# Kernel tuning notes

Hardware: AMD Instinct MI355X
Metric: run time of the kernel (lower is better)

Reference implementation:

```python
import jax
import jax.numpy as jnp
import numpy as np
from jax import lax

B, L, H, M = 32768, 128, 256, 16


def setup_inputs() -> dict:
    key = jax.random.key(0)
    ks = jax.random.split(key, 7)
    s_ih = 1.0 / np.sqrt(H)  # PyTorch GRUCell init scale (uniform bound); use scaled normal
    return {
        "x": jax.random.randint(ks[0], (B, L), 0, M, dtype=jnp.int32),
        "W_ih": jax.random.normal(ks[1], (3 * H, 1), dtype=jnp.float32) * s_ih,
        "W_hh": jax.random.normal(ks[2], (3 * H, H), dtype=jnp.float32) * s_ih,
        "b_ih": jax.random.normal(ks[3], (3 * H,), dtype=jnp.float32) * s_ih,
        "b_hh": jax.random.normal(ks[4], (3 * H,), dtype=jnp.float32) * s_ih,
        "W_fc": jax.random.normal(ks[5], (M, H), dtype=jnp.float32) * s_ih,
        "b_fc": jax.random.normal(ks[6], (M,), dtype=jnp.float32) * s_ih,
    }


def reference(x, W_ih, W_hh, b_ih, b_hh, W_fc, b_fc):
    # (zeros at i=0) as a scalar feature; output log_softmax gathered at x[:, i].
    xf = x.astype(jnp.float32)
    x_in = jnp.concatenate([jnp.zeros((x.shape[0], 1), jnp.float32), xf[:, :-1]], axis=1)  # [B, L]

    def step(h, inp):
        x_t, tgt = inp  # x_t: [B] float, tgt: [B] int
        gi = x_t[:, None] * W_ih.T + b_ih            # [B, 3H] (input dim is 1)
        gh = h @ W_hh.T + b_hh                       # [B, 3H]
        ir, iz, i_n = jnp.split(gi, 3, axis=1)
        hr, hz, h_n = jnp.split(gh, 3, axis=1)
        r = jax.nn.sigmoid(ir + hr)
        z = jax.nn.sigmoid(iz + hz)
        n = jnp.tanh(i_n + r * h_n)
        h_new = (1.0 - z) * n + z * h                # [B, H]
        logp = jax.nn.log_softmax(h_new @ W_fc.T + b_fc, axis=1)  # [B, M]
        lp = jnp.take_along_axis(logp, tgt[:, None], axis=1)[:, 0]  # [B]
        return h_new, lp

    h0 = jnp.zeros((x.shape[0], W_hh.shape[1]), jnp.float32)
    _, lps = lax.scan(step, h0, (x_in.T, x.T))  # lps: [L, B]
    return lps.sum(axis=0)  # [B] log_probsum
```

## Files before the change

### kernel.cpp

```cpp
#include <hip/hip_runtime.h>

typedef __attribute__((ext_vector_type(8))) short s16x8;
typedef __attribute__((ext_vector_type(4))) float f32x4;
typedef __attribute__((ext_vector_type(16))) float f32x16;

#define BATCH 32768
#define LSEQ 128
#define W32_SHORTS (8 * 4 * 17 * 512)
#define WFC_SHORTS 4096
#define XT_OFF_BYTES ((W32_SHORTS + WFC_SHORTS) * 2)
#define WS_NEED_XT (XT_OFF_BYTES + BATCH * LSEQ * 4)

#define HROW 264
#define HBUF_S (128 * HROW)
#define LDS_BYTES (2 * HBUF_S * 2 + 1024)

#define L2E 1.4426950408889634f
#define LN2 0.6931471805599453f

#define MFMA32(A, B, C) __builtin_amdgcn_mfma_f32_32x32x16_bf16(A, B, C, 0, 0, 0)
#define MFMA16(A, B, C) __builtin_amdgcn_mfma_f32_16x16x32_bf16(A, B, C, 0, 0, 0)

__device__ __forceinline__ unsigned short f2b(float f) {
  unsigned u = __float_as_uint(f);
  u += 0x7FFFu + ((u >> 16) & 1u);
  return (unsigned short)(u >> 16);
}

__device__ __forceinline__ float exp2n(float x) { float r; asm("v_exp_f32 %0, -%1" : "=v"(r) : "v"(x)); return r; }
__device__ __forceinline__ float exp2p(float x) { float r; asm("v_exp_f32 %0, %1" : "=v"(r) : "v"(x)); return r; }
__device__ __forceinline__ float rcp_(float x)  { float r; asm("v_rcp_f32 %0, %1" : "=v"(r) : "v"(x)); return r; }
__device__ __forceinline__ float log2_(float x) { float r; asm("v_log_f32 %0, %1" : "=v"(r) : "v"(x)); return r; }
__device__ __forceinline__ unsigned cvtpk(float lo, float hi) {
  unsigned r; asm("v_cvt_pk_bf16_f32 %0, %1, %2" : "=v"(r) : "v"(lo), "v"(hi)); return r;
}

__global__ void gru_prep(const float* __restrict__ Wih, const float* __restrict__ Whh,
                         const float* __restrict__ bih, const float* __restrict__ bhh,
                         const float* __restrict__ Wfc,
                         unsigned short* __restrict__ wfrag,
                         unsigned short* __restrict__ wfc16) {
  int t = blockIdx.x * 256 + threadIdx.x;
  if (t < W32_SHORTS) {
    int e = t & 7, lane = (t >> 3) & 63, frag = t >> 9;
    int ks = frag % 17, g = (frag / 17) & 3, tr = frag / 68;
    int l31 = lane & 31, hh = lane >> 5;
    int k = (ks < 16) ? ks * 16 + hh * 8 + e : 256 + hh * 8 + e;
    float val = 0.f;
    if (g < 3) {
      int j = g * 256 + tr * 32 + l31;
      if (k < 256) val = Whh[j * 256 + k];
      else if (k == 256) val = (g < 2) ? Wih[j] : 0.f;
      else if (k == 257) val = (g < 2) ? (bih[j] + bhh[j]) : bhh[j];
    }
    wfrag[t] = f2b(val);
  } else if (t < W32_SHORTS + WFC_SHORTS) {
    int t2 = t - W32_SHORTS;
    wfc16[t2] = f2b(Wfc[t2]);
  }
}

__global__ void x_transpose(const int* __restrict__ x, int* __restrict__ xT) {
  __shared__ int tile[32][33];
  int l0 = blockIdx.x * 32, b0 = blockIdx.y * 32;
  for (int r = threadIdx.y; r < 32; r += 8)
    tile[r][threadIdx.x] = x[(b0 + r) * LSEQ + l0 + threadIdx.x];
  __syncthreads();
  for (int r = threadIdx.y; r < 32; r += 8)
    xT[(l0 + r) * BATCH + b0 + threadIdx.x] = tile[threadIdx.x][r];
}

template <int XT>
__global__ __attribute__((amdgpu_waves_per_eu(2, 2))) __launch_bounds__(512)
void gru_main(const int* __restrict__ x, const int* __restrict__ xTr,
              const unsigned short* __restrict__ wfrag,
              const unsigned short* __restrict__ wfc16,
              const float* __restrict__ Wih, const float* __restrict__ bih,
              const float* __restrict__ bfc, float* __restrict__ out) {
  extern __shared__ unsigned short sm[];
  unsigned short* h0 = sm;
  unsigned short* h1 = sm + HBUF_S;
  unsigned* wl_in = (unsigned*)(sm + 2 * HBUF_S);

  const int tid = threadIdx.x;
  const int lane = tid & 63;
  const int wv = tid >> 6;
  const int tr = wv;
  const int l31 = lane & 31;
  const int hh = lane >> 5;
  const int q = lane >> 4;
  const int b = lane & 15;
  const int bbase = blockIdx.x * 128;

  {
    unsigned int* p = (unsigned int*)h0;
#pragma unroll
    for (int r = 0; r < 33; ++r) p[tid + r * 512] = 0u;
  }
  if (tid < 256) {
    int j = 512 + tid;
    wl_in[tid] = (unsigned)f2b(Wih[j]) | ((unsigned)f2b(bih[j]) << 16);
  }

  float bfc4[4];
#pragma unroll
  for (int r = 0; r < 4; ++r) bfc4[r] = bfc[q * 4 + r];

  const f32x16 z16 = {0, 0, 0, 0, 0, 0, 0, 0, 0, 0, 0, 0, 0, 0, 0, 0};

  float lp = 0.f;
  __syncthreads();

#pragma unroll 1
  for (int i = 0; i < LSEQ; ++i) {
    const unsigned short* rdb = (i & 1) ? h1 : h0;
    unsigned short* wrb = (i & 1) ? h0 : h1;

    unsigned long wfu = (unsigned long)wfrag;
    asm volatile("" : "+s"(wfu));
    const unsigned short* wfp = (const unsigned short*)wfu;
    unsigned long wcu = (unsigned long)wfc16;
    asm volatile("" : "+s"(wcu));
    const unsigned short* wc = (const unsigned short*)wcu;

    const unsigned short* fR = wfp + ((tr * 4 + 0) * 17) * 512 + lane * 8;
    const unsigned short* fZ = wfp + ((tr * 4 + 1) * 17) * 512 + lane * 8;
    const unsigned short* fH = wfp + ((tr * 4 + 2) * 17) * 512 + lane * 8;

    float xin4[4];
    unsigned xlo[4];
#pragma unroll
    for (int bg = 0; bg < 4; ++bg) {
      float xv;
      if (XT) xv = (i > 0) ? (float)xTr[(i - 1) * BATCH + bbase + bg * 32 + l31] : 0.f;
      else    xv = (i > 0) ? (float)x[(bbase + bg * 32 + l31) * LSEQ + i - 1] : 0.f;
      xin4[bg] = xv;
      xlo[bg] = (hh == 0) ? ((__float_as_uint(xv) >> 16) | 0x3F800000u) : 0u;
    }

    s16x8 ar = *(const s16x8*)(fR + 16 * 512);
    s16x8 az = *(const s16x8*)(fZ + 16 * 512);
    s16x8 ah = *(const s16x8*)(fH + 16 * 512);
    f32x16 aRc[4], aZc[4], aHc[4];
#pragma unroll
    for (int bg = 0; bg < 4; ++bg) {
      union { unsigned u[4]; s16x8 v; } xf;
      xf.u[0] = xlo[bg]; xf.u[1] = xf.u[2] = xf.u[3] = 0u;
      aRc[bg] = MFMA32(ar, xf.v, z16);
      aZc[bg] = MFMA32(az, xf.v, z16);
      aHc[bg] = MFMA32(ah, xf.v, z16);
    }

    const unsigned short* rbB = rdb + l31 * HROW + 8 * hh;

    s16x8 cr = *(const s16x8*)(fR);
    s16x8 cz = *(const s16x8*)(fZ);
    s16x8 ch = *(const s16x8*)(fH);
#pragma unroll
    for (int ks = 0; ks < 16; ++ks) {
      s16x8 nr, nz, nh;
      if (ks < 15) {
        nr = *(const s16x8*)(fR + (ks + 1) * 512);
        nz = *(const s16x8*)(fZ + (ks + 1) * 512);
        nh = *(const s16x8*)(fH + (ks + 1) * 512);
      }
#pragma unroll
      for (int bg = 0; bg < 4; ++bg) {
        const s16x8 hb = *(const s16x8*)&rbB[bg * 32 * HROW + ks * 16];
        aRc[bg] = MFMA32(cr, hb, aRc[bg]);
        aZc[bg] = MFMA32(cz, hb, aZc[bg]);
        aHc[bg] = MFMA32(ch, hb, aHc[bg]);
      }
      if (ks < 15) { cr = nr; cz = nz; ch = nh; }
    }

    const unsigned short* rbE = rdb + l31 * HROW + tr * 32 + 4 * hh;
    unsigned short* wbE = wrb + l31 * HROW + tr * 32 + 4 * hh;
    const unsigned* wlt = wl_in + tr * 32 + 4 * hh;
#pragma unroll
    for (int bg = 0; bg < 4; ++bg) {
      const float xv = xin4[bg];
#pragma unroll
      for (int rq = 0; rq < 4; ++rq) {
        const uint2 hp = *(const uint2*)&rbE[bg * 32 * HROW + 8 * rq];
        const float hpv[4] = {
            __uint_as_float(hp.x << 16), __uint_as_float(hp.x & 0xFFFF0000u),
            __uint_as_float(hp.y << 16), __uint_as_float(hp.y & 0xFFFF0000u)};
        float hv[4];
#pragma unroll
        for (int e2 = 0; e2 < 4; ++e2) {
          const int idx = rq * 4 + e2;
          const unsigned u = wlt[8 * rq + e2];
          const float inr = fmaf(xv, __uint_as_float(u << 16),
                                 __uint_as_float(u & 0xFFFF0000u));
          float rr = rcp_(1.f + exp2n(L2E * aRc[bg][idx]));
          float zz = rcp_(1.f + exp2n(L2E * aZc[bg][idx]));
          float y  = fmaf(rr, aHc[bg][idx], inr);
          float uu = rcp_(1.f + exp2p((2.f * L2E) * y));
          float nn = fmaf(-2.f, uu, 1.f);
          hv[e2] = fmaf(zz, hpv[e2] - nn, nn);
        }
        *(uint2*)&wbE[bg * 32 * HROW + 8 * rq] =
            make_uint2(cvtpk(hv[0], hv[1]), cvtpk(hv[2], hv[3]));
      }
    }

    __syncthreads();

    {
      const int lrow = wv * 16 + b;
      const int grow = bbase + lrow;
      f32x4 fa = {bfc4[0], bfc4[1], bfc4[2], bfc4[3]};
      const unsigned short* hbb = wrb + lrow * HROW + 8 * q;
      const unsigned short* wcb = wc + b * 256 + q * 8;
#pragma unroll
      for (int ks = 0; ks < 8; ++ks) {
        s16x8 wfcf = *(const s16x8*)(wcb + 32 * ks);
        s16x8 hb = *(const s16x8*)(hbb + 32 * ks);
        fa = MFMA16(wfcf, hb, fa);
      }
      int tgt = XT ? xTr[i * BATCH + grow] : x[grow * LSEQ + i];
      float l0 = fa[0], l1 = fa[1], l2 = fa[2], l3 = fa[3];
      float mx = fmaxf(fmaxf(l0, l1), fmaxf(l2, l3));
      mx = fmaxf(mx, __shfl_xor(mx, 16));
      mx = fmaxf(mx, __shfl_xor(mx, 32));
      float se = exp2p(L2E * (l0 - mx)) + exp2p(L2E * (l1 - mx)) +
                 exp2p(L2E * (l2 - mx)) + exp2p(L2E * (l3 - mx));
      se += __shfl_xor(se, 16);
      se += __shfl_xor(se, 32);
      float v01 = (tgt & 1) ? l1 : l0;
      float v23 = (tgt & 1) ? l3 : l2;
      float vs = (tgt & 2) ? v23 : v01;
      float contrib = (q == (tgt >> 2)) ? vs : 0.f;
      contrib += __shfl_xor(contrib, 16);
      contrib += __shfl_xor(contrib, 32);
      lp += contrib - mx - LN2 * log2_(se);
    }
  }

  if (q == 0) out[bbase + wv * 16 + b] = lp;
}

extern "C" void kernel_launch(void* const* d_in, const int* in_sizes, int n_in,
                              void* d_out, int out_size, void* d_ws, size_t ws_size,
                              hipStream_t stream) {
  (void)in_sizes; (void)n_in; (void)out_size;
  const int*   x   = (const int*)d_in[0];
  const float* Wih = (const float*)d_in[1];
  const float* Whh = (const float*)d_in[2];
  const float* bih = (const float*)d_in[3];
  const float* bhh = (const float*)d_in[4];
  const float* Wfc = (const float*)d_in[5];
  const float* bfc = (const float*)d_in[6];
  float* out = (float*)d_out;

  unsigned short* wfrag = (unsigned short*)d_ws;
  unsigned short* wfc16 = wfrag + W32_SHORTS;
  int* xT = (int*)((char*)d_ws + XT_OFF_BYTES);

  gru_prep<<<dim3((W32_SHORTS + WFC_SHORTS) / 256), dim3(256), 0, stream>>>(
      Wih, Whh, bih, bhh, Wfc, wfrag, wfc16);

  if (ws_size >= (size_t)WS_NEED_XT) {
    x_transpose<<<dim3(LSEQ / 32, BATCH / 32), dim3(32, 8), 0, stream>>>(x, xT);
    hipFuncSetAttribute((const void*)gru_main<1>,
                        hipFuncAttributeMaxDynamicSharedMemorySize, LDS_BYTES);
    gru_main<1><<<dim3(256), dim3(512), LDS_BYTES, stream>>>(x, xT, wfrag, wfc16,
                                                             Wih, bih, bfc, out);
  } else {
    hipFuncSetAttribute((const void*)gru_main<0>,
                        hipFuncAttributeMaxDynamicSharedMemorySize, LDS_BYTES);
    gru_main<0><<<dim3(256), dim3(512), LDS_BYTES, stream>>>(x, x, wfrag, wfc16,
                                                             Wih, bih, bfc, out);
  }
}
```

Before: 2.187 ms.

## Halve batch rows per block to double blocks and raise waves per EU

Each block now handles 64 batch rows instead of 128, so 512 blocks are launched and the per-wave accumulator set shrinks from 12 to 6 f32x16 tiles. This lets the waves_per_eu hint rise from 2 to 4, and the weight prefetch double-buffering is dropped so register pressure falls. The aim is better latency hiding through higher occupancy in the serial recurrence. In exchange, the W_hh fragments are reloaded from global/L2 twice as often per batch row. Only half the waves do the output-projection and softmax phase.

```diff
diff --git a/kernel.cpp b/kernel.cpp
--- a/kernel.cpp
+++ b/kernel.cpp
@@ -11,9 +11,10 @@
 #define XT_OFF_BYTES ((W32_SHORTS + WFC_SHORTS) * 2)
 #define WS_NEED_XT (XT_OFF_BYTES + BATCH * LSEQ * 4)
 
+#define BROWS 64
 #define HROW 264
-#define HBUF_S (128 * HROW)
-#define LDS_BYTES (2 * HBUF_S * 2 + 1024)
+#define HBUF_S (BROWS * HROW)
+#define LDS_BYTES (2 * HBUF_S * 2 + 256 * 4 + 16 * 4)
 
 #define L2E 1.4426950408889634f
 #define LN2 0.6931471805599453f
@@ -71,7 +72,7 @@
 }
 
 template <int XT>
-__global__ __attribute__((amdgpu_waves_per_eu(2, 2))) __launch_bounds__(512)
+__global__ __attribute__((amdgpu_waves_per_eu(4, 4))) __launch_bounds__(512)
 void gru_main(const int* __restrict__ x, const int* __restrict__ xTr,
               const unsigned short* __restrict__ wfrag,
               const unsigned short* __restrict__ wfc16,
@@ -81,6 +82,7 @@
   unsigned short* h0 = sm;
   unsigned short* h1 = sm + HBUF_S;
   unsigned* wl_in = (unsigned*)(sm + 2 * HBUF_S);
+  float* bfcl = (float*)(wl_in + 256);
 
   const int tid = threadIdx.x;
   const int lane = tid & 63;
@@ -90,21 +92,19 @@
   const int hh = lane >> 5;
   const int q = lane >> 4;
   const int b = lane & 15;
-  const int bbase = blockIdx.x * 128;
+  const int bbase = blockIdx.x * BROWS;
 
   {
     unsigned int* p = (unsigned int*)h0;
 #pragma unroll
-    for (int r = 0; r < 33; ++r) p[tid + r * 512] = 0u;
+    for (int r = 0; r < 16; ++r) p[tid + r * 512] = 0u;
+    if (tid < 256) p[tid + 16 * 512] = 0u;
   }
   if (tid < 256) {
     int j = 512 + tid;
     wl_in[tid] = (unsigned)f2b(Wih[j]) | ((unsigned)f2b(bih[j]) << 16);
   }
-
-  float bfc4[4];
-#pragma unroll
-  for (int r = 0; r < 4; ++r) bfc4[r] = bfc[q * 4 + r];
+  if (tid < 16) bfcl[tid] = bfc[tid];
 
   const f32x16 z16 = {0, 0, 0, 0, 0, 0, 0, 0, 0, 0, 0, 0, 0, 0, 0, 0};
 
@@ -127,90 +127,85 @@
     const unsigned short* fZ = wfp + ((tr * 4 + 1) * 17) * 512 + lane * 8;
     const unsigned short* fH = wfp + ((tr * 4 + 2) * 17) * 512 + lane * 8;
 
-    float xin4[4];
-    unsigned xlo[4];
-#pragma unroll
-    for (int bg = 0; bg < 4; ++bg) {
-      float xv;
-      if (XT) xv = (i > 0) ? (float)xTr[(i - 1) * BATCH + bbase + bg * 32 + l31] : 0.f;
-      else    xv = (i > 0) ? (float)x[(bbase + bg * 32 + l31) * LSEQ + i - 1] : 0.f;
-      xin4[bg] = xv;
-      xlo[bg] = (hh == 0) ? ((__float_as_uint(xv) >> 16) | 0x3F800000u) : 0u;
-    }
-
-    s16x8 ar = *(const s16x8*)(fR + 16 * 512);
-    s16x8 az = *(const s16x8*)(fZ + 16 * 512);
-    s16x8 ah = *(const s16x8*)(fH + 16 * 512);
-    f32x16 aRc[4], aZc[4], aHc[4];
-#pragma unroll
-    for (int bg = 0; bg < 4; ++bg) {
-      union { unsigned u[4]; s16x8 v; } xf;
-      xf.u[0] = xlo[bg]; xf.u[1] = xf.u[2] = xf.u[3] = 0u;
-      aRc[bg] = MFMA32(ar, xf.v, z16);
-      aZc[bg] = MFMA32(az, xf.v, z16);
-      aHc[bg] = MFMA32(ah, xf.v, z16);
+    float xv0, xv1;
+    if (XT) {
+      xv0 = (i > 0) ? (float)xTr[(i - 1) * BATCH + bbase + l31] : 0.f;
+      xv1 = (i > 0) ? (float)xTr[(i - 1) * BATCH + bbase + 32 + l31] : 0.f;
+    } else {
+      xv0 = (i > 0) ? (float)x[(bbase + l31) * LSEQ + i - 1] : 0.f;
+      xv1 = (i > 0) ? (float)x[(bbase + 32 + l31) * LSEQ + i - 1] : 0.f;
+    }
+
+    f32x16 aR0, aR1, aZ0, aZ1, aH0, aH1;
+    {
+      union { unsigned u[4]; s16x8 v; } xf0, xf1;
+      xf0.u[0] = (hh == 0) ? ((__float_as_uint(xv0) >> 16) | 0x3F800000u) : 0u;
+      xf0.u[1] = xf0.u[2] = xf0.u[3] = 0u;
+      xf1.u[0] = (hh == 0) ? ((__float_as_uint(xv1) >> 16) | 0x3F800000u) : 0u;
+      xf1.u[1] = xf1.u[2] = xf1.u[3] = 0u;
+      s16x8 w;
+      w = *(const s16x8*)(fR + 16 * 512);
+      aR0 = MFMA32(w, xf0.v, z16); aR1 = MFMA32(w, xf1.v, z16);
+      w = *(const s16x8*)(fZ + 16 * 512);
+      aZ0 = MFMA32(w, xf0.v, z16); aZ1 = MFMA32(w, xf1.v, z16);
+      w = *(const s16x8*)(fH + 16 * 512);
+      aH0 = MFMA32(w, xf0.v, z16); aH1 = MFMA32(w, xf1.v, z16);
     }
 
     const unsigned short* rbB = rdb + l31 * HROW + 8 * hh;
 
-    s16x8 cr = *(const s16x8*)(fR);
-    s16x8 cz = *(const s16x8*)(fZ);
-    s16x8 ch = *(const s16x8*)(fH);
 #pragma unroll
     for (int ks = 0; ks < 16; ++ks) {
-      s16x8 nr, nz, nh;
-      if (ks < 15) {
-        nr = *(const s16x8*)(fR + (ks + 1) * 512);
-        nz = *(const s16x8*)(fZ + (ks + 1) * 512);
-        nh = *(const s16x8*)(fH + (ks + 1) * 512);
-      }
-#pragma unroll
-      for (int bg = 0; bg < 4; ++bg) {
-        const s16x8 hb = *(const s16x8*)&rbB[bg * 32 * HROW + ks * 16];
-        aRc[bg] = MFMA32(cr, hb, aRc[bg]);
-        aZc[bg] = MFMA32(cz, hb, aZc[bg]);
-        aHc[bg] = MFMA32(ch, hb, aHc[bg]);
-      }
-      if (ks < 15) { cr = nr; cz = nz; ch = nh; }
-    }
-
-    const unsigned short* rbE = rdb + l31 * HROW + tr * 32 + 4 * hh;
-    unsigned short* wbE = wrb + l31 * HROW + tr * 32 + 4 * hh;
+      const s16x8 hb0 = *(const s16x8*)&rbB[0 * 32 * HROW + ks * 16];
+      const s16x8 hb1 = *(const s16x8*)&rbB[1 * 32 * HROW + ks * 16];
+      s16x8 w;
+      w = *(const s16x8*)(fR + ks * 512);
+      aR0 = MFMA32(w, hb0, aR0); aR1 = MFMA32(w, hb1, aR1);
+      w = *(const s16x8*)(fZ + ks * 512);
+      aZ0 = MFMA32(w, hb0, aZ0); aZ1 = MFMA32(w, hb1, aZ1);
+      w = *(const s16x8*)(fH + ks * 512);
+      aH0 = MFMA32(w, hb0, aH0); aH1 = MFMA32(w, hb1, aH1);
+    }
+
     const unsigned* wlt = wl_in + tr * 32 + 4 * hh;
-#pragma unroll
-    for (int bg = 0; bg < 4; ++bg) {
-      const float xv = xin4[bg];
-#pragma unroll
-      for (int rq = 0; rq < 4; ++rq) {
-        const uint2 hp = *(const uint2*)&rbE[bg * 32 * HROW + 8 * rq];
-        const float hpv[4] = {
-            __uint_as_float(hp.x << 16), __uint_as_float(hp.x & 0xFFFF0000u),
-            __uint_as_float(hp.y << 16), __uint_as_float(hp.y & 0xFFFF0000u)};
-        float hv[4];
-#pragma unroll
-        for (int e2 = 0; e2 < 4; ++e2) {
-          const int idx = rq * 4 + e2;
-          const unsigned u = wlt[8 * rq + e2];
-          const float inr = fmaf(xv, __uint_as_float(u << 16),
-                                 __uint_as_float(u & 0xFFFF0000u));
-          float rr = rcp_(1.f + exp2n(L2E * aRc[bg][idx]));
-          float zz = rcp_(1.f + exp2n(L2E * aZc[bg][idx]));
-          float y  = fmaf(rr, aHc[bg][idx], inr);
-          float uu = rcp_(1.f + exp2p((2.f * L2E) * y));
-          float nn = fmaf(-2.f, uu, 1.f);
-          hv[e2] = fmaf(zz, hpv[e2] - nn, nn);
-        }
-        *(uint2*)&wbE[bg * 32 * HROW + 8 * rq] =
-            make_uint2(cvtpk(hv[0], hv[1]), cvtpk(hv[2], hv[3]));
-      }
-    }
+#define EPI(AR, AZ, AH, BG, XV)                                                 \
+    {                                                                           \
+      const int rowb = ((BG) * 32 + l31) * HROW;                                \
+      _Pragma("unroll")                                                         \
+      for (int rq = 0; rq < 4; ++rq) {                                          \
+        const int col = tr * 32 + 4 * hh + 8 * rq;                              \
+        const uint2 hp = *(const uint2*)&rdb[rowb + col];                       \
+        const float hpv[4] = {                                                  \
+            __uint_as_float(hp.x << 16), __uint_as_float(hp.x & 0xFFFF0000u),   \
+            __uint_as_float(hp.y << 16), __uint_as_float(hp.y & 0xFFFF0000u)};  \
+        float hv[4];                                                            \
+        _Pragma("unroll")                                                       \
+        for (int e2 = 0; e2 < 4; ++e2) {                                        \
+          const int idx = rq * 4 + e2;                                          \
+          const unsigned u = wlt[8 * rq + e2];                                  \
+          const float inr = fmaf((XV), __uint_as_float(u << 16),                \
+                                 __uint_as_float(u & 0xFFFF0000u));             \
+          float rr = rcp_(1.f + exp2n(L2E * (AR)[idx]));                        \
+          float zz = rcp_(1.f + exp2n(L2E * (AZ)[idx]));                        \
+          float y  = fmaf(rr, (AH)[idx], inr);                                  \
+          float uu = rcp_(1.f + exp2p((2.f * L2E) * y));                        \
+          float nn = fmaf(-2.f, uu, 1.f);                                       \
+          hv[e2] = fmaf(zz, hpv[e2] - nn, nn);                                  \
+        }                                                                       \
+        *(uint2*)&wrb[rowb + col] =                                             \
+            make_uint2(cvtpk(hv[0], hv[1]), cvtpk(hv[2], hv[3]));               \
+      }                                                                         \
+    }
+    EPI(aR0, aZ0, aH0, 0, xv0)
+    EPI(aR1, aZ1, aH1, 1, xv1)
+#undef EPI
 
     __syncthreads();
 
-    {
+    if (wv < 4) {
       const int lrow = wv * 16 + b;
       const int grow = bbase + lrow;
-      f32x4 fa = {bfc4[0], bfc4[1], bfc4[2], bfc4[3]};
+      f32x4 fa = {bfcl[q * 4 + 0], bfcl[q * 4 + 1], bfcl[q * 4 + 2], bfcl[q * 4 + 3]};
       const unsigned short* hbb = wrb + lrow * HROW + 8 * q;
       const unsigned short* wcb = wc + b * 256 + q * 8;
 #pragma unroll
@@ -238,7 +233,7 @@
     }
   }
 
-  if (q == 0) out[bbase + wv * 16 + b] = lp;
+  if (wv < 4 && q == 0) out[bbase + wv * 16 + b] = lp;
 }
 
 extern "C" void kernel_launch(void* const* d_in, const int* in_sizes, int n_in,
@@ -265,12 +260,12 @@
     x_transpose<<<dim3(LSEQ / 32, BATCH / 32), dim3(32, 8), 0, stream>>>(x, xT);
     hipFuncSetAttribute((const void*)gru_main<1>,
                         hipFuncAttributeMaxDynamicSharedMemorySize, LDS_BYTES);
-    gru_main<1><<<dim3(256), dim3(512), LDS_BYTES, stream>>>(x, xT, wfrag, wfc16,
-                                                             Wih, bih, bfc, out);
+    gru_main<1><<<dim3(BATCH / BROWS), dim3(512), LDS_BYTES, stream>>>(
+        x, xT, wfrag, wfc16, Wih, bih, bfc, out);
   } else {
     hipFuncSetAttribute((const void*)gru_main<0>,
                         hipFuncAttributeMaxDynamicSharedMemorySize, LDS_BYTES);
-    gru_main<0><<<dim3(256), dim3(512), LDS_BYTES, stream>>>(x, x, wfrag, wfc16,
-                                                             Wih, bih, bfc, out);
-  }
-}
+    gru_main<0><<<dim3(BATCH / BROWS), dim3(512), LDS_BYTES, stream>>>(
+        x, x, wfrag, wfc16, Wih, bih, bfc, out);
+  }
+}
```

After: 7.606 ms. 248% more time.
